# Optimization experiments

Hardware: AMD Instinct MI355X
Metric: run time of the kernel (lower is better)

Reference implementation:

```python
import jax, jax.numpy as jnp
import numpy as np

B, L, D = 1, 2048, 512
NL, N, K = 4, 16, 4
DI = 2 * D          # mamba expand=2
R = D // 16         # dt_rank = ceil(D/16)
H = 4 * D           # mlp hidden


def _ln(x, w, b, eps=1e-5):
    mu = x.mean(-1, keepdims=True)
    v = ((x - mu) ** 2).mean(-1, keepdims=True)
    return (x - mu) * jax.lax.rsqrt(v + eps) * w + b


def _rms(x, w, eps=1e-5):
    return x * jax.lax.rsqrt((x * x).mean(-1, keepdims=True) + eps) * w


def _ssm_scan(delta, Bm, Cm, u, A, Dp):
    # delta,u: (B,L,DI); Bm,Cm: (B,L,N); A: (DI,N); Dp: (DI,)
    def step(h, inp):
        d_t, b_t, c_t, u_t = inp                              # (B,DI),(B,N),(B,N),(B,DI)
        dA = jnp.exp(d_t[..., None] * A)                      # (B,DI,N)
        h = dA * h + (d_t * u_t)[..., None] * b_t[:, None, :]
        y = jnp.einsum('bdn,bn->bd', h, c_t)
        return h, y
    h0 = jnp.zeros((delta.shape[0], DI, N), delta.dtype)
    xs = (delta.swapaxes(0, 1), Bm.swapaxes(0, 1), Cm.swapaxes(0, 1), u.swapaxes(0, 1))
    _, ys = jax.lax.scan(step, h0, xs)
    return ys.swapaxes(0, 1) + u * Dp


def _mamba(h, in_w, cw, cb, xw, dtw, dtb, A_log, Dp, ow):
    xz = h @ in_w.T                                           # (B,L,2*DI)
    x, z = jnp.split(xz, 2, axis=-1)
    # causal depthwise conv1d, kernel K, left pad K-1
    xp = jnp.pad(x, ((0, 0), (K - 1, 0), (0, 0)))
    Ls = x.shape[1]
    x = sum(cw[:, k] * xp[:, k:k + Ls, :] for k in range(K)) + cb
    x = jax.nn.silu(x)
    dbc = x @ xw.T                                            # (B,L,R+2N)
    dt, Bm, Cm = dbc[..., :R], dbc[..., R:R + N], dbc[..., R + N:]
    delta = jax.nn.softplus(dt @ dtw.T + dtb)                 # (B,L,DI)
    A = -jnp.exp(A_log)                                       # (DI,N)
    y = _ssm_scan(delta, Bm, Cm, x, A, Dp)
    y = y * jax.nn.silu(z)
    return y @ ow.T


def _forward(hidden_states, ln1_w, ln1_b, in_proj_w, conv_w, conv_b, x_proj_w,
             dt_proj_w, dt_proj_b, A_log, D_param, out_proj_w, block_norm_w,
             norm_f_w, ln2_w, ln2_b, fc1_w, fc1_b, fc2_w, fc2_b):
    shortcut = hidden_states
    h = _ln(hidden_states, ln1_w, ln1_b)
    residual = None
    for i in range(in_proj_w.shape[0]):
        residual = h if residual is None else h + residual    # residual_in_fp32
        hn = _rms(residual, block_norm_w[i])                  # fused_add_norm prenorm
        h = _mamba(hn, in_proj_w[i], conv_w[i], conv_b[i], x_proj_w[i],
                   dt_proj_w[i], dt_proj_b[i], A_log[i], D_param[i], out_proj_w[i])
    h = _rms(h + residual, norm_f_w)                          # final rms_norm_fn
    h = shortcut + h
    x = _ln(h, ln2_w, ln2_b)
    x = jax.nn.gelu(x @ fc1_w.T + fc1_b)
    x = x @ fc2_w.T + fc2_b
    return h + x


def setup_inputs() -> dict:
    key = jax.random.key(0)
    ks = jax.random.split(key, 9)
    s = 0.02
    return {
        'hidden_states': jax.random.normal(ks[0], (B, L, D), jnp.float32),
        'ln1_w': jnp.ones((D,), jnp.float32),
        'ln1_b': jnp.zeros((D,), jnp.float32),
        'in_proj_w': jax.random.normal(ks[1], (NL, 2 * DI, D), jnp.float32) * s,
        'conv_w': jax.random.normal(ks[2], (NL, DI, K), jnp.float32) * 0.3,
        'conv_b': jnp.zeros((NL, DI), jnp.float32),
        'x_proj_w': jax.random.normal(ks[3], (NL, R + 2 * N, DI), jnp.float32) * s,
        'dt_proj_w': jax.random.normal(ks[4], (NL, DI, R), jnp.float32) * s,
        'dt_proj_b': jax.random.uniform(ks[5], (NL, DI), jnp.float32, -4.0, -2.0),
        'A_log': jnp.tile(jnp.log(jnp.arange(1, N + 1, dtype=jnp.float32)), (NL, DI, 1)),
        'D_param': jnp.ones((NL, DI), jnp.float32),
        'out_proj_w': jax.random.normal(ks[6], (NL, D, DI), jnp.float32) * s,
        'block_norm_w': jnp.ones((NL, D), jnp.float32),
        'norm_f_w': jnp.ones((D,), jnp.float32),
        'ln2_w': jnp.ones((D,), jnp.float32),
        'ln2_b': jnp.zeros((D,), jnp.float32),
        'fc1_w': jax.random.normal(ks[7], (H, D), jnp.float32) * s,
        'fc1_b': jnp.zeros((H,), jnp.float32),
        'fc2_w': jax.random.normal(ks[8], (D, H), jnp.float32) * s,
        'fc2_b': jnp.zeros((D,), jnp.float32),
    }


def reference(hidden_states, ln1_w, ln1_b, in_proj_w, conv_w, conv_b, x_proj_w,
              dt_proj_w, dt_proj_b, A_log, D_param, out_proj_w, block_norm_w,
              norm_f_w, ln2_w, ln2_b, fc1_w, fc1_b, fc2_w, fc2_b):
    return _forward(hidden_states, ln1_w, ln1_b, in_proj_w, conv_w, conv_b,
                    x_proj_w, dt_proj_w, dt_proj_b, A_log, D_param, out_proj_w,
                    block_norm_w, norm_f_w, ln2_w, ln2_b, fc1_w, fc1_b, fc2_w, fc2_b)
```

## Files before the change

kernel.cpp:

```cpp
#include <hip/hip_runtime.h>
#include <hip/hip_bf16.h>
#include <math.h>

#define L_SEQ 2048
#define Dm    512
#define DI    1024
#define Nst   16
#define Kc    4
#define Rr    32
#define NL    4
#define CH    128
#define LC    (L_SEQ / CH)

typedef __attribute__((ext_vector_type(8))) short bf16x8;
typedef __attribute__((ext_vector_type(4))) float f32x4;

__device__ __forceinline__ float act_softplus(float x) {
    return fmaxf(x, 0.f) + log1pf(__expf(-fabsf(x)));
}
__device__ __forceinline__ float act_gelu(float x) {
    float c = 0.7978845608028654f * (x + 0.044715f * x * x * x);
    float t = 1.f - 2.f / (__expf(2.f * c) + 1.f);
    return 0.5f * x * (1.f + t);
}
__device__ __forceinline__ float silu_(float x) {
    return x / (1.f + __expf(-x));
}
__device__ __forceinline__ ushort f2bf(float f) {
    union { float f; unsigned u; } c; c.f = f;
    unsigned r = c.u + 0x7fffu + ((c.u >> 16) & 1u);
    return (ushort)(r >> 16);
}
__device__ __forceinline__ float bf2f(ushort u) {
    union { unsigned u; float f; } c; c.u = ((unsigned)u) << 16;
    return c.f;
}
__device__ __forceinline__ float wave_sum(float v) {
    #pragma unroll
    for (int off = 32; off; off >>= 1) v += __shfl_xor(v, off);
    return v;
}

__global__ __launch_bounds__(256) void cast_all_kernel(
    const float* __restrict__ s0, ushort* __restrict__ d0, int n0,
    const float* __restrict__ s1, ushort* __restrict__ d1, int n1,
    const float* __restrict__ s2, ushort* __restrict__ d2, int n2,
    const float* __restrict__ s3, ushort* __restrict__ d3, int n3,
    const float* __restrict__ s4, ushort* __restrict__ d4, int n4_,
    const float* __restrict__ s5, ushort* __restrict__ d5, int n5)
{
    int i = blockIdx.x * 256 + threadIdx.x;
    const float* s; ushort* d;
    if (i < n0) { s = s0; d = d0; }
    else { i -= n0; if (i < n1) { s = s1; d = d1; }
    else { i -= n1; if (i < n2) { s = s2; d = d2; }
    else { i -= n2; if (i < n3) { s = s3; d = d3; }
    else { i -= n3; if (i < n4_) { s = s4; d = d4; }
    else { i -= n4_; if (i < n5) { s = s5; d = d5; } else return; } } } } }
    float4 v = ((const float4*)s)[i];
    ushort4 o;
    o.x = f2bf(v.x); o.y = f2bf(v.y); o.z = f2bf(v.z); o.w = f2bf(v.w);
    ((ushort4*)d)[i] = o;
}

__global__ __launch_bounds__(256) void ln_rms_kernel(const float* __restrict__ x,
    const float* __restrict__ w, const float* __restrict__ b,
    const float* __restrict__ rw, float* __restrict__ res,
    ushort* __restrict__ hn_bf)
{
    int lane = threadIdx.x & 63, wv = threadIdx.x >> 6;
    int row = blockIdx.x * 4 + wv;
    size_t base = (size_t)row * Dm + lane * 8;
    float v[8];
    *(float4*)(v)     = *(const float4*)(x + base);
    *(float4*)(v + 4) = *(const float4*)(x + base + 4);
    float s = 0.f, ss = 0.f;
    #pragma unroll
    for (int q = 0; q < 8; ++q) { s += v[q]; ss += v[q] * v[q]; }
    s = wave_sum(s); ss = wave_sum(ss);
    float mu = s * (1.f / Dm);
    float rs = rsqrtf(ss * (1.f / Dm) - mu * mu + 1e-5f);
    float wv8[8], bv8[8], rv8[8];
    *(float4*)(wv8)     = *(const float4*)(w + lane * 8);
    *(float4*)(wv8 + 4) = *(const float4*)(w + lane * 8 + 4);
    *(float4*)(bv8)     = *(const float4*)(b + lane * 8);
    *(float4*)(bv8 + 4) = *(const float4*)(b + lane * 8 + 4);
    *(float4*)(rv8)     = *(const float4*)(rw + lane * 8);
    *(float4*)(rv8 + 4) = *(const float4*)(rw + lane * 8 + 4);
    float o[8], ss2 = 0.f;
    #pragma unroll
    for (int q = 0; q < 8; ++q) {
        o[q] = (v[q] - mu) * rs * wv8[q] + bv8[q];
        ss2 += o[q] * o[q];
    }
    *(float4*)(res + base)     = *(float4*)(o);
    *(float4*)(res + base + 4) = *(float4*)(o + 4);
    ss2 = wave_sum(ss2);
    float rr = rsqrtf(ss2 * (1.f / Dm) + 1e-5f);
    bf16x8 hb;
    #pragma unroll
    for (int q = 0; q < 8; ++q) hb[q] = (short)f2bf(o[q] * rr * rv8[q]);
    *(bf16x8*)(hn_bf + base) = hb;
}

__global__ __launch_bounds__(256) void add_rms_kernel(const ushort* __restrict__ hb,
    float* __restrict__ res, const float* __restrict__ w, ushort* __restrict__ rms_out)
{
    int lane = threadIdx.x & 63, wv = threadIdx.x >> 6;
    int row = blockIdx.x * 4 + wv;
    size_t base = (size_t)row * Dm + lane * 8;
    bf16x8 hv = *(const bf16x8*)(hb + base);
    float v[8];
    *(float4*)(v)     = *(const float4*)(res + base);
    *(float4*)(v + 4) = *(const float4*)(res + base + 4);
    float ss = 0.f;
    #pragma unroll
    for (int q = 0; q < 8; ++q) {
        v[q] += bf2f((ushort)hv[q]);
        ss += v[q] * v[q];
    }
    *(float4*)(res + base)     = *(float4*)(v);
    *(float4*)(res + base + 4) = *(float4*)(v + 4);
    ss = wave_sum(ss);
    float rr = rsqrtf(ss * (1.f / Dm) + 1e-5f);
    float wv8[8];
    *(float4*)(wv8)     = *(const float4*)(w + lane * 8);
    *(float4*)(wv8 + 4) = *(const float4*)(w + lane * 8 + 4);
    bf16x8 ob;
    #pragma unroll
    for (int q = 0; q < 8; ++q) ob[q] = (short)f2bf(v[q] * rr * wv8[q]);
    *(bf16x8*)(rms_out + base) = ob;
}

__global__ __launch_bounds__(256) void final_ln2_kernel(const ushort* __restrict__ hb,
    const float* __restrict__ res, const float* __restrict__ shortcut,
    const float* __restrict__ wf, const float* __restrict__ w2,
    const float* __restrict__ b2, float* __restrict__ hout,
    ushort* __restrict__ yb16)
{
    int lane = threadIdx.x & 63, wv = threadIdx.x >> 6;
    int row = blockIdx.x * 4 + wv;
    size_t base = (size_t)row * Dm + lane * 8;
    bf16x8 hv = *(const bf16x8*)(hb + base);
    float v[8];
    *(float4*)(v)     = *(const float4*)(res + base);
    *(float4*)(v + 4) = *(const float4*)(res + base + 4);
    float ss = 0.f;
    #pragma unroll
    for (int q = 0; q < 8; ++q) {
        v[q] += bf2f((ushort)hv[q]);
        ss += v[q] * v[q];
    }
    ss = wave_sum(ss);
    float rs = rsqrtf(ss * (1.f / Dm) + 1e-5f);
    float sc[8], wf8[8];
    *(float4*)(sc)     = *(const float4*)(shortcut + base);
    *(float4*)(sc + 4) = *(const float4*)(shortcut + base + 4);
    *(float4*)(wf8)     = *(const float4*)(wf + lane * 8);
    *(float4*)(wf8 + 4) = *(const float4*)(wf + lane * 8 + 4);
    float t[8], s2 = 0.f, ss2 = 0.f;
    #pragma unroll
    for (int q = 0; q < 8; ++q) {
        t[q] = sc[q] + v[q] * rs * wf8[q];
        s2 += t[q]; ss2 += t[q] * t[q];
    }
    *(float4*)(hout + base)     = *(float4*)(t);
    *(float4*)(hout + base + 4) = *(float4*)(t + 4);
    s2 = wave_sum(s2); ss2 = wave_sum(ss2);
    float mu = s2 * (1.f / Dm);
    float rsig = rsqrtf(ss2 * (1.f / Dm) - mu * mu + 1e-5f);
    float w28[8], b28[8];
    *(float4*)(w28)     = *(const float4*)(w2 + lane * 8);
    *(float4*)(w28 + 4) = *(const float4*)(w2 + lane * 8 + 4);
    *(float4*)(b28)     = *(const float4*)(b2 + lane * 8);
    *(float4*)(b28 + 4) = *(const float4*)(b2 + lane * 8 + 4);
    bf16x8 ob;
    #pragma unroll
    for (int q = 0; q < 8; ++q) ob[q] = (short)f2bf((t[q] - mu) * rsig * w28[q] + b28[q]);
    *(bf16x8*)(yb16 + base) = ob;
}

template<int BM, int BN, int BK, int EPI>
__global__ __launch_bounds__(256) void gemm_mfma(
    const ushort* __restrict__ A, int lda,
    const ushort* __restrict__ W, int K,
    void* __restrict__ Cout, int ldc,
    const float* __restrict__ bias, const float* __restrict__ addsrc)
{
    constexpr int ROWB  = BK * 2;
    constexpr int SMASK = (ROWB / 16) - 1;
    constexpr int KK    = BK / 32;
    constexpr int WM = BM / 2, WN = BN / 2;
    constexpr int FM = WM / 16, FN = WN / 16;
    constexpr int ISS_A = (BM * ROWB) / 4096;
    constexpr int ISS_W = (BN * ROWB) / 4096;

    __shared__ __align__(16) ushort As[BM * BK];
    __shared__ __align__(16) ushort Ws[BN * BK];

    int tid = threadIdx.x;
    int wave = tid >> 6, lane = tid & 63;
    int wr = wave >> 1, wc = wave & 1;
    int l16 = lane & 15, lk = lane >> 4;
    int bm = blockIdx.y * BM, bn = blockIdx.x * BN;

    const ushort* srcA[ISS_A];
    const ushort* srcW[ISS_W];
    #pragma unroll
    for (int s = 0; s < ISS_A; ++s) {
        int off = s * 4096 + wave * 1024 + lane * 16;
        int row = off / ROWB;
        int slot = (off % ROWB) >> 4;
        int col = ((slot ^ (row & SMASK)) << 3);
        srcA[s] = A + (size_t)(bm + row) * lda + col;
    }
    #pragma unroll
    for (int s = 0; s < ISS_W; ++s) {
        int off = s * 4096 + wave * 1024 + lane * 16;
        int row = off / ROWB;
        int slot = (off % ROWB) >> 4;
        int col = ((slot ^ (row & SMASK)) << 3);
        srcW[s] = W + (size_t)(bn + row) * K + col;
    }
    int aoff[FM][KK], woff[FN][KK];
    #pragma unroll
    for (int i = 0; i < FM; ++i) {
        int row = wr * WM + i * 16 + l16;
        #pragma unroll
        for (int kk = 0; kk < KK; ++kk)
            aoff[i][kk] = row * BK + ((((kk << 2) | lk) ^ (row & SMASK)) << 3);
    }
    #pragma unroll
    for (int j = 0; j < FN; ++j) {
        int row = wc * WN + j * 16 + l16;
        #pragma unroll
        for (int kk = 0; kk < KK; ++kk)
            woff[j][kk] = row * BK + ((((kk << 2) | lk) ^ (row & SMASK)) << 3);
    }

    f32x4 acc[FM][FN] = {};

    for (int k0 = 0; k0 < K; k0 += BK) {
        #pragma unroll
        for (int s = 0; s < ISS_A; ++s)
            __builtin_amdgcn_global_load_lds(
                (const __attribute__((address_space(1))) void*)(srcA[s] + k0),
                (__attribute__((address_space(3))) void*)((char*)As + s * 4096 + wave * 1024),
                16, 0, 0);
        #pragma unroll
        for (int s = 0; s < ISS_W; ++s)
            __builtin_amdgcn_global_load_lds(
                (const __attribute__((address_space(1))) void*)(srcW[s] + k0),
                (__attribute__((address_space(3))) void*)((char*)Ws + s * 4096 + wave * 1024),
                16, 0, 0);
        __syncthreads();
        #pragma unroll
        for (int kk = 0; kk < KK; ++kk) {
            bf16x8 af[FM], wf[FN];
            #pragma unroll
            for (int i = 0; i < FM; ++i) af[i] = *(const bf16x8*)(As + aoff[i][kk]);
            #pragma unroll
            for (int j = 0; j < FN; ++j) wf[j] = *(const bf16x8*)(Ws + woff[j][kk]);
            #pragma unroll
            for (int i = 0; i < FM; ++i)
                #pragma unroll
                for (int j = 0; j < FN; ++j)
                    acc[i][j] = __builtin_amdgcn_mfma_f32_16x16x32_bf16(af[i], wf[j], acc[i][j], 0, 0, 0);
        }
        __syncthreads();
    }

    int orow0 = bm + wr * WM, ocol0 = bn + wc * WN;
    #pragma unroll
    for (int j = 0; j < FN; ++j) {
        int col = ocol0 + j * 16 + l16;
        float bj = 0.f;
        if constexpr (EPI == 2 || EPI == 4) bj = bias[col];
        #pragma unroll
        for (int i = 0; i < FM; ++i) {
            #pragma unroll
            for (int r = 0; r < 4; ++r) {
                int row = orow0 + i * 16 + lk * 4 + r;
                float v = acc[i][j][r];
                if constexpr (EPI == 1) {
                    ((ushort*)Cout)[(size_t)row * ldc + col] = f2bf(v);
                } else if constexpr (EPI == 2) {
                    ((ushort*)Cout)[(size_t)row * ldc + col] = f2bf(act_gelu(v + bj));
                } else if constexpr (EPI == 4) {
                    ((float*)Cout)[(size_t)row * ldc + col] = v + bj + addsrc[(size_t)row * ldc + col];
                }
            }
        }
    }
}

__global__ __launch_bounds__(256) void xproj_conv_kernel(
    const ushort* __restrict__ xz, const float* __restrict__ cw,
    const float* __restrict__ cb, const ushort* __restrict__ W,
    ushort* __restrict__ xc, float* __restrict__ part)
{
    constexpr int BM = 64, BN = 64, BK = 64;
    constexpr int ROWB  = BK * 2;
    constexpr int SMASK = (ROWB / 16) - 1;
    constexpr int KK    = BK / 32;
    constexpr int WM = 32, WN = 32, FM = 2, FN = 2;

    __shared__ __align__(16) ushort As[BM * BK];
    __shared__ __align__(16) ushort Ws[BN * BK];

    int tid = threadIdx.x;
    int wave = tid >> 6, lane = tid & 63;
    int wr = wave >> 1, wc = wave & 1;
    int l16 = lane & 15, lk = lane >> 4;
    int bm = blockIdx.y * BM;
    int z = blockIdx.z;
    int kbeg = z * (DI / 4);

    const ushort* srcW[2];
    #pragma unroll
    for (int s = 0; s < 2; ++s) {
        int off = s * 4096 + wave * 1024 + lane * 16;
        int row = off / ROWB;
        int slot = (off % ROWB) >> 4;
        int col = ((slot ^ (row & SMASK)) << 3);
        srcW[s] = W + (size_t)row * DI + kbeg + col;
    }
    int aoff[FM][KK], woff[FN][KK];
    #pragma unroll
    for (int i = 0; i < FM; ++i) {
        int row = wr * WM + i * 16 + l16;
        #pragma unroll
        for (int kk = 0; kk < KK; ++kk)
            aoff[i][kk] = row * BK + ((((kk << 2) | lk) ^ (row & SMASK)) << 3);
    }
    #pragma unroll
    for (int j = 0; j < FN; ++j) {
        int row = wc * WN + j * 16 + l16;
        #pragma unroll
        for (int kk = 0; kk < KK; ++kk)
            woff[j][kk] = row * BK + ((((kk << 2) | lk) ^ (row & SMASK)) << 3);
    }

    f32x4 acc[FM][FN] = {};

    for (int k0 = 0; k0 < DI / 4; k0 += BK) {
        #pragma unroll
        for (int s = 0; s < 2; ++s)
            __builtin_amdgcn_global_load_lds(
                (const __attribute__((address_space(1))) void*)(srcW[s] + k0),
                (__attribute__((address_space(3))) void*)((char*)Ws + s * 4096 + wave * 1024),
                16, 0, 0);
        #pragma unroll
        for (int s = 0; s < 2; ++s) {
            int off = s * 4096 + wave * 1024 + lane * 16;
            int row = off >> 7;
            int slot = (off >> 4) & 7;
            int t = bm + row;
            int dcol = kbeg + k0 + slot * 8;
            float a[8];
            float4 c4[8];
            #pragma unroll
            for (int q = 0; q < 8; ++q) {
                a[q] = cb[dcol + q];
                c4[q] = *(const float4*)(cw + (size_t)(dcol + q) * 4);
            }
            #pragma unroll
            for (int k = 0; k < 4; ++k) {
                int tt = t + k - 3;
                if (tt >= 0) {
                    bf16x8 xv = *(const bf16x8*)(xz + (size_t)tt * (2 * DI) + dcol);
                    #pragma unroll
                    for (int q = 0; q < 8; ++q) {
                        float wk = (k == 0) ? c4[q].x : (k == 1) ? c4[q].y
                                 : (k == 2) ? c4[q].z : c4[q].w;
                        a[q] = fmaf(wk, bf2f((ushort)xv[q]), a[q]);
                    }
                }
            }
            bf16x8 o;
            #pragma unroll
            for (int q = 0; q < 8; ++q) o[q] = (short)f2bf(silu_(a[q]));
            *(bf16x8*)(xc + (size_t)t * DI + dcol) = o;
            *(bf16x8*)(As + row * BK + ((slot ^ (row & SMASK)) << 3)) = o;
        }
        __syncthreads();
        #pragma unroll
        for (int kk = 0; kk < KK; ++kk) {
            bf16x8 af[FM], wf[FN];
            #pragma unroll
            for (int i = 0; i < FM; ++i) af[i] = *(const bf16x8*)(As + aoff[i][kk]);
            #pragma unroll
            for (int j = 0; j < FN; ++j) wf[j] = *(const bf16x8*)(Ws + woff[j][kk]);
            #pragma unroll
            for (int i = 0; i < FM; ++i)
                #pragma unroll
                for (int j = 0; j < FN; ++j)
                    acc[i][j] = __builtin_amdgcn_mfma_f32_16x16x32_bf16(af[i], wf[j], acc[i][j], 0, 0, 0);
        }
        __syncthreads();
    }

    float* coutf = part + (size_t)z * L_SEQ * 64;
    int orow0 = bm + wr * WM, ocol0 = wc * WN;
    #pragma unroll
    for (int j = 0; j < FN; ++j) {
        int col = ocol0 + j * 16 + l16;
        #pragma unroll
        for (int i = 0; i < FM; ++i)
            #pragma unroll
            for (int r = 0; r < 4; ++r) {
                int row = orow0 + i * 16 + lk * 4 + r;
                coutf[(size_t)row * 64 + col] = acc[i][j][r];
            }
    }
}

__global__ __launch_bounds__(256) void scan_chunk_kernel(
    const float* __restrict__ part, const ushort* __restrict__ u,
    const ushort* __restrict__ wdt, const float* __restrict__ dtb,
    const float* __restrict__ A_log,
    float* __restrict__ hend, float* __restrict__ aprod)
{
    __shared__ float sdt[LC][32];
    __shared__ float bsm[LC][16];
    int tid = threadIdx.x;
    int c = blockIdx.x;
    int d = blockIdx.y * 256 + tid;
    int t0 = c * LC;
    const int S = L_SEQ * 64;
    for (int i = tid; i < LC * 48; i += 256) {
        int tt = i / 48, cc = i % 48;
        int idx = (t0 + tt) * 64 + cc;
        float s = part[idx] + part[idx + S] + part[idx + 2 * S] + part[idx + 3 * S];
        if (cc < 32) sdt[tt][cc] = s; else bsm[tt][cc - 32] = s;
    }
    bf16x8 wd[4];
    #pragma unroll
    for (int p = 0; p < 4; ++p) wd[p] = *(const bf16x8*)(wdt + (size_t)d * 32 + p * 8);
    float bd = dtb[d];
    float A2[16];
    {
        float a[16];
        #pragma unroll
        for (int q = 0; q < 4; ++q)
            *(float4*)(a + q * 4) = ((const float4*)(A_log + (size_t)d * 16))[q];
        #pragma unroll
        for (int n = 0; n < 16; ++n)
            A2[n] = -__expf(a[n]) * 1.44269504f;
    }
    float h[16], ap[16];
    #pragma unroll
    for (int n = 0; n < 16; ++n) { h[n] = 0.f; ap[n] = 1.f; }
    __syncthreads();
    for (int tt = 0; tt < LC; ++tt) {
        int t = t0 + tt;
        float dtv = bd;
        #pragma unroll
        for (int p = 0; p < 4; ++p)
            #pragma unroll
            for (int e = 0; e < 8; ++e)
                dtv = fmaf(sdt[tt][p * 8 + e], bf2f((ushort)wd[p][e]), dtv);
        dtv = act_softplus(dtv);
        float du = dtv * bf2f(u[(size_t)t * DI + d]);
        #pragma unroll
        for (int n = 0; n < 16; ++n) {
            float dA = exp2f(dtv * A2[n]);
            h[n] = fmaf(dA, h[n], du * bsm[tt][n]);
            ap[n] *= dA;
        }
    }
    size_t base = ((size_t)c * DI + d) * 16;
    #pragma unroll
    for (int q = 0; q < 4; ++q) {
        ((float4*)(hend + base))[q]  = *(float4*)(h + q * 4);
        ((float4*)(aprod + base))[q] = *(float4*)(ap + q * 4);
    }
}

__global__ __launch_bounds__(64) void chunk_prefix_kernel(
    const float* __restrict__ hend, float* __restrict__ aprod_hin)
{
    int j = blockIdx.x * 64 + threadIdx.x;
    float h = 0.f;
    for (int cg = 0; cg < CH; cg += 8) {
        float ap[8], he[8];
        #pragma unroll
        for (int q = 0; q < 8; ++q) {
            size_t o = (size_t)(cg + q) * (DI * Nst) + j;
            ap[q] = aprod_hin[o]; he[q] = hend[o];
        }
        #pragma unroll
        for (int q = 0; q < 8; ++q) {
            size_t o = (size_t)(cg + q) * (DI * Nst) + j;
            aprod_hin[o] = h;
            h = fmaf(ap[q], h, he[q]);
        }
    }
}

__global__ __launch_bounds__(256) void scan_apply_kernel(
    const float* __restrict__ part, const ushort* __restrict__ u,
    const ushort* __restrict__ wdt, const float* __restrict__ dtb,
    const float* __restrict__ A_log, const float* __restrict__ Dp,
    const ushort* __restrict__ xz, const float* __restrict__ hin,
    ushort* __restrict__ y)
{
    __shared__ float sdt[LC][32];
    __shared__ float bsm[LC][16], csm[LC][16];
    int tid = threadIdx.x;
    int c = blockIdx.x;
    int d = blockIdx.y * 256 + tid;
    int t0 = c * LC;
    const int S = L_SEQ * 64;
    for (int i = tid; i < LC * 64; i += 256) {
        int tt = i >> 6, cc = i & 63;
        int idx = (t0 + tt) * 64 + cc;
        float s = part[idx] + part[idx + S] + part[idx + 2 * S] + part[idx + 3 * S];
        if (cc < 32) sdt[tt][cc] = s;
        else if (cc < 48) bsm[tt][cc - 32] = s;
        else csm[tt][cc - 48] = s;
    }
    bf16x8 wd[4];
    #pragma unroll
    for (int p = 0; p < 4; ++p) wd[p] = *(const bf16x8*)(wdt + (size_t)d * 32 + p * 8);
    float bd = dtb[d];
    float A2[16];
    {
        float a[16];
        #pragma unroll
        for (int q = 0; q < 4; ++q)
            *(float4*)(a + q * 4) = ((const float4*)(A_log + (size_t)d * 16))[q];
        #pragma unroll
        for (int n = 0; n < 16; ++n)
            A2[n] = -__expf(a[n]) * 1.44269504f;
    }
    float h[16];
    size_t base = ((size_t)c * DI + d) * 16;
    #pragma unroll
    for (int q = 0; q < 4; ++q)
        *(float4*)(h + q * 4) = ((const float4*)(hin + base))[q];
    float Dval = Dp[d];
    __syncthreads();
    for (int tt = 0; tt < LC; ++tt) {
        int t = t0 + tt;
        float dtv = bd;
        #pragma unroll
        for (int p = 0; p < 4; ++p)
            #pragma unroll
            for (int e = 0; e < 8; ++e)
                dtv = fmaf(sdt[tt][p * 8 + e], bf2f((ushort)wd[p][e]), dtv);
        dtv = act_softplus(dtv);
        float u_ = bf2f(u[(size_t)t * DI + d]);
        float du = dtv * u_;
        float acc = 0.f;
        #pragma unroll
        for (int n = 0; n < 16; ++n) {
            float dA = exp2f(dtv * A2[n]);
            h[n] = fmaf(dA, h[n], du * bsm[tt][n]);
            acc = fmaf(h[n], csm[tt][n], acc);
        }
        float zv = bf2f(xz[(size_t)t * (2 * DI) + DI + d]);
        y[(size_t)t * DI + d] = f2bf((acc + u_ * Dval) * silu_(zv));
    }
}

extern "C" void kernel_launch(void* const* d_in, const int* in_sizes, int n_in,
                              void* d_out, int out_size, void* d_ws, size_t ws_size,
                              hipStream_t stream)
{
    const float* hidden     = (const float*)d_in[0];
    const float* ln1_w      = (const float*)d_in[1];
    const float* ln1_b      = (const float*)d_in[2];
    const float* in_proj_w  = (const float*)d_in[3];
    const float* conv_w     = (const float*)d_in[4];
    const float* conv_b     = (const float*)d_in[5];
    const float* x_proj_w   = (const float*)d_in[6];
    const float* dt_proj_w  = (const float*)d_in[7];
    const float* dt_proj_b  = (const float*)d_in[8];
    const float* A_log      = (const float*)d_in[9];
    const float* D_param    = (const float*)d_in[10];
    const float* out_proj_w = (const float*)d_in[11];
    const float* block_norm_w = (const float*)d_in[12];
    const float* norm_f_w   = (const float*)d_in[13];
    const float* ln2_w      = (const float*)d_in[14];
    const float* ln2_b      = (const float*)d_in[15];
    const float* fc1_w      = (const float*)d_in[16];
    const float* fc1_b      = (const float*)d_in[17];
    const float* fc2_w      = (const float*)d_in[18];
    const float* fc2_b      = (const float*)d_in[19];

    char* P = (char*)d_ws;
    auto alloc = [&](size_t bytes) { char* r = P; P += (bytes + 255) & ~(size_t)255; return r; };
    float* hout   = (float*)alloc((size_t)L_SEQ * Dm * 4);
    float* res    = (float*)alloc((size_t)L_SEQ * Dm * 4);
    float* part   = (float*)alloc((size_t)4 * L_SEQ * 64 * 4);
    float* hend   = (float*)alloc((size_t)CH * DI * Nst * 4);
    float* aprod  = (float*)alloc((size_t)CH * DI * Nst * 4);
    ushort* h_bf  = (ushort*)alloc((size_t)L_SEQ * Dm * 2);
    ushort* hn_bf = (ushort*)alloc((size_t)L_SEQ * Dm * 2);
    ushort* xz_bf = (ushort*)alloc((size_t)L_SEQ * 2 * DI * 2);
    ushort* xc_bf = (ushort*)alloc((size_t)L_SEQ * DI * 2);
    ushort* yb_bf = (ushort*)alloc((size_t)L_SEQ * DI * 2);
    ushort* w_in  = (ushort*)alloc((size_t)NL * 2 * DI * Dm * 2);
    ushort* w_out = (ushort*)alloc((size_t)NL * Dm * DI * 2);
    ushort* w_x   = (ushort*)alloc((size_t)NL * 64 * DI * 2);
    ushort* w_dt  = (ushort*)alloc((size_t)NL * DI * Rr * 2);
    ushort* w_fc1 = (ushort*)alloc((size_t)(4 * Dm) * Dm * 2);
    ushort* w_fc2 = (ushort*)alloc((size_t)Dm * (4 * Dm) * 2);
    float* out  = (float*)d_out;

    {
        int n0 = NL * 2 * DI * Dm / 4, n1 = NL * Dm * DI / 4, n2 = NL * 64 * DI / 4;
        int n3 = NL * DI * Rr / 4, n4_ = 4 * Dm * Dm / 4, n5 = Dm * 4 * Dm / 4;
        int tot = n0 + n1 + n2 + n3 + n4_ + n5;
        cast_all_kernel<<<(tot + 255) / 256, 256, 0, stream>>>(
            in_proj_w, w_in, n0, out_proj_w, w_out, n1, x_proj_w, w_x, n2,
            dt_proj_w, w_dt, n3, fc1_w, w_fc1, n4_, fc2_w, w_fc2, n5);
    }

    ln_rms_kernel<<<L_SEQ / 4, 256, 0, stream>>>(hidden, ln1_w, ln1_b,
                                                 block_norm_w, res, hn_bf);

    dim3 gscan(CH, DI / 256);
    for (int i = 0; i < NL; ++i) {
        if (i) add_rms_kernel<<<L_SEQ / 4, 256, 0, stream>>>(h_bf, res,
                                                  block_norm_w + i * Dm, hn_bf);
        gemm_mfma<128, 128, 128, 1><<<dim3(2 * DI / 128, L_SEQ / 128), 256, 0, stream>>>(
            hn_bf, Dm, w_in + (size_t)i * 2 * DI * Dm, Dm, xz_bf, 2 * DI, nullptr, nullptr);
        xproj_conv_kernel<<<dim3(1, L_SEQ / 64, 4), 256, 0, stream>>>(
            xz_bf, conv_w + i * DI * Kc, conv_b + i * DI,
            w_x + (size_t)i * 64 * DI, xc_bf, part);
        scan_chunk_kernel<<<gscan, 256, 0, stream>>>(part, xc_bf,
                                        w_dt + (size_t)i * DI * Rr, dt_proj_b + i * DI,
                                        A_log + (size_t)i * DI * Nst, hend, aprod);
        chunk_prefix_kernel<<<(DI * Nst) / 64, 64, 0, stream>>>(hend, aprod);
        scan_apply_kernel<<<gscan, 256, 0, stream>>>(part, xc_bf,
                                        w_dt + (size_t)i * DI * Rr, dt_proj_b + i * DI,
                                        A_log + (size_t)i * DI * Nst,
                                        D_param + i * DI, xz_bf, aprod, yb_bf);
        gemm_mfma<64, 64, 128, 1><<<dim3(Dm / 64, L_SEQ / 64), 256, 0, stream>>>(
            yb_bf, DI, w_out + (size_t)i * Dm * DI, DI, h_bf, Dm, nullptr, nullptr);
    }

    final_ln2_kernel<<<L_SEQ / 4, 256, 0, stream>>>(h_bf, res, hidden, norm_f_w,
                                                ln2_w, ln2_b, hout, hn_bf);
    gemm_mfma<128, 128, 128, 2><<<dim3(2048 / 128, L_SEQ / 128), 256, 0, stream>>>(
        hn_bf, Dm, w_fc1, Dm, xz_bf, 2048, fc1_b, nullptr);
    gemm_mfma<64, 64, 128, 4><<<dim3(Dm / 64, L_SEQ / 64), 256, 0, stream>>>(
        xz_bf, 2048, w_fc2, 2048, out, Dm, fc2_b, hout);
}
```

Baseline: 476.7 us.

## Fuse LN into cast kernel, cache delta, raise x_proj split-K, shrink GEMM tiles

Merges the initial layernorm/RMS kernel into the weight-cast launch, which saves one kernel launch. The scan-chunk pass now writes softplus(delta) in bf16 so that scan_apply reads it instead of recomputing the dt projection. The x_proj split-K factor goes from 4 to 8 to spread the work over more blocks. GEMM tile N sizes are halved to raise block counts. The costs are extra partial-sum traffic, a delta buffer write and read, and bf16 rounding of delta in both scan passes.

New measurement: 390.5 us (median of 2 runs). -18.1%, faster.

```diff
diff --git a/kernel.cpp b/kernel.cpp
--- a/kernel.cpp
+++ b/kernel.cpp
@@ -11,6 +11,7 @@
 #define NL    4
 #define CH    128
 #define LC    (L_SEQ / CH)
+#define KSX   8
 
 typedef __attribute__((ext_vector_type(8))) short bf16x8;
 typedef __attribute__((ext_vector_type(4))) float f32x4;
@@ -41,15 +42,54 @@
     return v;
 }
 
-__global__ __launch_bounds__(256) void cast_all_kernel(
+__global__ __launch_bounds__(256) void setup_kernel(
     const float* __restrict__ s0, ushort* __restrict__ d0, int n0,
     const float* __restrict__ s1, ushort* __restrict__ d1, int n1,
     const float* __restrict__ s2, ushort* __restrict__ d2, int n2,
     const float* __restrict__ s3, ushort* __restrict__ d3, int n3,
     const float* __restrict__ s4, ushort* __restrict__ d4, int n4_,
-    const float* __restrict__ s5, ushort* __restrict__ d5, int n5)
-{
-    int i = blockIdx.x * 256 + threadIdx.x;
+    const float* __restrict__ s5, ushort* __restrict__ d5, int n5,
+    const float* __restrict__ x, const float* __restrict__ w,
+    const float* __restrict__ b, const float* __restrict__ rw,
+    float* __restrict__ res, ushort* __restrict__ hn_bf)
+{
+    if (blockIdx.x < 512) {
+        int lane = threadIdx.x & 63, wv = threadIdx.x >> 6;
+        int row = blockIdx.x * 4 + wv;
+        size_t base = (size_t)row * Dm + lane * 8;
+        float v[8];
+        *(float4*)(v)     = *(const float4*)(x + base);
+        *(float4*)(v + 4) = *(const float4*)(x + base + 4);
+        float s = 0.f, ss = 0.f;
+        #pragma unroll
+        for (int q = 0; q < 8; ++q) { s += v[q]; ss += v[q] * v[q]; }
+        s = wave_sum(s); ss = wave_sum(ss);
+        float mu = s * (1.f / Dm);
+        float rs = rsqrtf(ss * (1.f / Dm) - mu * mu + 1e-5f);
+        float wv8[8], bv8[8], rv8[8];
+        *(float4*)(wv8)     = *(const float4*)(w + lane * 8);
+        *(float4*)(wv8 + 4) = *(const float4*)(w + lane * 8 + 4);
+        *(float4*)(bv8)     = *(const float4*)(b + lane * 8);
+        *(float4*)(bv8 + 4) = *(const float4*)(b + lane * 8 + 4);
+        *(float4*)(rv8)     = *(const float4*)(rw + lane * 8);
+        *(float4*)(rv8 + 4) = *(const float4*)(rw + lane * 8 + 4);
+        float o[8], ss2 = 0.f;
+        #pragma unroll
+        for (int q = 0; q < 8; ++q) {
+            o[q] = (v[q] - mu) * rs * wv8[q] + bv8[q];
+            ss2 += o[q] * o[q];
+        }
+        *(float4*)(res + base)     = *(float4*)(o);
+        *(float4*)(res + base + 4) = *(float4*)(o + 4);
+        ss2 = wave_sum(ss2);
+        float rr = rsqrtf(ss2 * (1.f / Dm) + 1e-5f);
+        bf16x8 hb;
+        #pragma unroll
+        for (int q = 0; q < 8; ++q) hb[q] = (short)f2bf(o[q] * rr * rv8[q]);
+        *(bf16x8*)(hn_bf + base) = hb;
+        return;
+    }
+    int i = (blockIdx.x - 512) * 256 + threadIdx.x;
     const float* s; ushort* d;
     if (i < n0) { s = s0; d = d0; }
     else { i -= n0; if (i < n1) { s = s1; d = d1; }
@@ -63,46 +103,6 @@
     ((ushort4*)d)[i] = o;
 }
 
-__global__ __launch_bounds__(256) void ln_rms_kernel(const float* __restrict__ x,
-    const float* __restrict__ w, const float* __restrict__ b,
-    const float* __restrict__ rw, float* __restrict__ res,
-    ushort* __restrict__ hn_bf)
-{
-    int lane = threadIdx.x & 63, wv = threadIdx.x >> 6;
-    int row = blockIdx.x * 4 + wv;
-    size_t base = (size_t)row * Dm + lane * 8;
-    float v[8];
-    *(float4*)(v)     = *(const float4*)(x + base);
-    *(float4*)(v + 4) = *(const float4*)(x + base + 4);
-    float s = 0.f, ss = 0.f;
-    #pragma unroll
-    for (int q = 0; q < 8; ++q) { s += v[q]; ss += v[q] * v[q]; }
-    s = wave_sum(s); ss = wave_sum(ss);
-    float mu = s * (1.f / Dm);
-    float rs = rsqrtf(ss * (1.f / Dm) - mu * mu + 1e-5f);
-    float wv8[8], bv8[8], rv8[8];
-    *(float4*)(wv8)     = *(const float4*)(w + lane * 8);
-    *(float4*)(wv8 + 4) = *(const float4*)(w + lane * 8 + 4);
-    *(float4*)(bv8)     = *(const float4*)(b + lane * 8);
-    *(float4*)(bv8 + 4) = *(const float4*)(b + lane * 8 + 4);
-    *(float4*)(rv8)     = *(const float4*)(rw + lane * 8);
-    *(float4*)(rv8 + 4) = *(const float4*)(rw + lane * 8 + 4);
-    float o[8], ss2 = 0.f;
-    #pragma unroll
-    for (int q = 0; q < 8; ++q) {
-        o[q] = (v[q] - mu) * rs * wv8[q] + bv8[q];
-        ss2 += o[q] * o[q];
-    }
-    *(float4*)(res + base)     = *(float4*)(o);
-    *(float4*)(res + base + 4) = *(float4*)(o + 4);
-    ss2 = wave_sum(ss2);
-    float rr = rsqrtf(ss2 * (1.f / Dm) + 1e-5f);
-    bf16x8 hb;
-    #pragma unroll
-    for (int q = 0; q < 8; ++q) hb[q] = (short)f2bf(o[q] * rr * rv8[q]);
-    *(bf16x8*)(hn_bf + base) = hb;
-}
-
 __global__ __launch_bounds__(256) void add_rms_kernel(const ushort* __restrict__ hb,
     float* __restrict__ res, const float* __restrict__ w, ushort* __restrict__ rms_out)
 {
@@ -314,7 +314,7 @@
     int l16 = lane & 15, lk = lane >> 4;
     int bm = blockIdx.y * BM;
     int z = blockIdx.z;
-    int kbeg = z * (DI / 4);
+    int kbeg = z * (DI / KSX);
 
     const ushort* srcW[2];
     #pragma unroll
@@ -343,7 +343,7 @@
 
     f32x4 acc[FM][FN] = {};
 
-    for (int k0 = 0; k0 < DI / 4; k0 += BK) {
+    for (int k0 = 0; k0 < DI / KSX; k0 += BK) {
         #pragma unroll
         for (int s = 0; s < 2; ++s)
             __builtin_amdgcn_global_load_lds(
@@ -419,7 +419,8 @@
     const float* __restrict__ part, const ushort* __restrict__ u,
     const ushort* __restrict__ wdt, const float* __restrict__ dtb,
     const float* __restrict__ A_log,
-    float* __restrict__ hend, float* __restrict__ aprod)
+    float* __restrict__ hend, float* __restrict__ aprod,
+    ushort* __restrict__ delta_bf)
 {
     __shared__ float sdt[LC][32];
     __shared__ float bsm[LC][16];
@@ -431,7 +432,9 @@
     for (int i = tid; i < LC * 48; i += 256) {
         int tt = i / 48, cc = i % 48;
         int idx = (t0 + tt) * 64 + cc;
-        float s = part[idx] + part[idx + S] + part[idx + 2 * S] + part[idx + 3 * S];
+        float s = 0.f;
+        #pragma unroll
+        for (int p = 0; p < KSX; ++p) s += part[idx + p * S];
         if (cc < 32) sdt[tt][cc] = s; else bsm[tt][cc - 32] = s;
     }
     bf16x8 wd[4];
@@ -460,11 +463,13 @@
             #pragma unroll
             for (int e = 0; e < 8; ++e)
                 dtv = fmaf(sdt[tt][p * 8 + e], bf2f((ushort)wd[p][e]), dtv);
-        dtv = act_softplus(dtv);
-        float du = dtv * bf2f(u[(size_t)t * DI + d]);
+        ushort dbf = f2bf(act_softplus(dtv));
+        delta_bf[(size_t)t * DI + d] = dbf;
+        float dt_ = bf2f(dbf);
+        float du = dt_ * bf2f(u[(size_t)t * DI + d]);
         #pragma unroll
         for (int n = 0; n < 16; ++n) {
-            float dA = exp2f(dtv * A2[n]);
+            float dA = exp2f(dt_ * A2[n]);
             h[n] = fmaf(dA, h[n], du * bsm[tt][n]);
             ap[n] *= dA;
         }
@@ -499,31 +504,25 @@
 }
 
 __global__ __launch_bounds__(256) void scan_apply_kernel(
-    const float* __restrict__ part, const ushort* __restrict__ u,
-    const ushort* __restrict__ wdt, const float* __restrict__ dtb,
-    const float* __restrict__ A_log, const float* __restrict__ Dp,
-    const ushort* __restrict__ xz, const float* __restrict__ hin,
-    ushort* __restrict__ y)
-{
-    __shared__ float sdt[LC][32];
+    const float* __restrict__ part, const ushort* __restrict__ delta,
+    const ushort* __restrict__ u, const float* __restrict__ A_log,
+    const float* __restrict__ Dp, const ushort* __restrict__ xz,
+    const float* __restrict__ hin, ushort* __restrict__ y)
+{
     __shared__ float bsm[LC][16], csm[LC][16];
     int tid = threadIdx.x;
     int c = blockIdx.x;
     int d = blockIdx.y * 256 + tid;
     int t0 = c * LC;
     const int S = L_SEQ * 64;
-    for (int i = tid; i < LC * 64; i += 256) {
-        int tt = i >> 6, cc = i & 63;
-        int idx = (t0 + tt) * 64 + cc;
-        float s = part[idx] + part[idx + S] + part[idx + 2 * S] + part[idx + 3 * S];
-        if (cc < 32) sdt[tt][cc] = s;
-        else if (cc < 48) bsm[tt][cc - 32] = s;
-        else csm[tt][cc - 48] = s;
-    }
-    bf16x8 wd[4];
-    #pragma unroll
-    for (int p = 0; p < 4; ++p) wd[p] = *(const bf16x8*)(wdt + (size_t)d * 32 + p * 8);
-    float bd = dtb[d];
+    for (int i = tid; i < LC * 32; i += 256) {
+        int tt = i >> 5, k = i & 31;
+        int idx = (t0 + tt) * 64 + 32 + k;
+        float s = 0.f;
+        #pragma unroll
+        for (int p = 0; p < KSX; ++p) s += part[idx + p * S];
+        if (k < 16) bsm[tt][k] = s; else csm[tt][k - 16] = s;
+    }
     float A2[16];
     {
         float a[16];
@@ -543,19 +542,13 @@
     __syncthreads();
     for (int tt = 0; tt < LC; ++tt) {
         int t = t0 + tt;
-        float dtv = bd;
-        #pragma unroll
-        for (int p = 0; p < 4; ++p)
-            #pragma unroll
-            for (int e = 0; e < 8; ++e)
-                dtv = fmaf(sdt[tt][p * 8 + e], bf2f((ushort)wd[p][e]), dtv);
-        dtv = act_softplus(dtv);
-        float u_ = bf2f(u[(size_t)t * DI + d]);
-        float du = dtv * u_;
+        float dt_ = bf2f(delta[(size_t)t * DI + d]);
+        float u_  = bf2f(u[(size_t)t * DI + d]);
+        float du  = dt_ * u_;
         float acc = 0.f;
         #pragma unroll
         for (int n = 0; n < 16; ++n) {
-            float dA = exp2f(dtv * A2[n]);
+            float dA = exp2f(dt_ * A2[n]);
             h[n] = fmaf(dA, h[n], du * bsm[tt][n]);
             acc = fmaf(h[n], csm[tt][n], acc);
         }
@@ -593,10 +586,11 @@
     auto alloc = [&](size_t bytes) { char* r = P; P += (bytes + 255) & ~(size_t)255; return r; };
     float* hout   = (float*)alloc((size_t)L_SEQ * Dm * 4);
     float* res    = (float*)alloc((size_t)L_SEQ * Dm * 4);
-    float* part   = (float*)alloc((size_t)4 * L_SEQ * 64 * 4);
+    float* part   = (float*)alloc((size_t)KSX * L_SEQ * 64 * 4);
     float* hend   = (float*)alloc((size_t)CH * DI * Nst * 4);
     float* aprod  = (float*)alloc((size_t)CH * DI * Nst * 4);
     ushort* h_bf  = (ushort*)alloc((size_t)L_SEQ * Dm * 2);
+    ushort* delta_bf = (ushort*)alloc((size_t)L_SEQ * DI * 2);
     ushort* hn_bf = (ushort*)alloc((size_t)L_SEQ * Dm * 2);
     ushort* xz_bf = (ushort*)alloc((size_t)L_SEQ * 2 * DI * 2);
     ushort* xc_bf = (ushort*)alloc((size_t)L_SEQ * DI * 2);
@@ -613,39 +607,37 @@
         int n0 = NL * 2 * DI * Dm / 4, n1 = NL * Dm * DI / 4, n2 = NL * 64 * DI / 4;
         int n3 = NL * DI * Rr / 4, n4_ = 4 * Dm * Dm / 4, n5 = Dm * 4 * Dm / 4;
         int tot = n0 + n1 + n2 + n3 + n4_ + n5;
-        cast_all_kernel<<<(tot + 255) / 256, 256, 0, stream>>>(
+        int grid = 512 + (tot + 255) / 256;
+        setup_kernel<<<grid, 256, 0, stream>>>(
             in_proj_w, w_in, n0, out_proj_w, w_out, n1, x_proj_w, w_x, n2,
-            dt_proj_w, w_dt, n3, fc1_w, w_fc1, n4_, fc2_w, w_fc2, n5);
-    }
-
-    ln_rms_kernel<<<L_SEQ / 4, 256, 0, stream>>>(hidden, ln1_w, ln1_b,
-                                                 block_norm_w, res, hn_bf);
+            dt_proj_w, w_dt, n3, fc1_w, w_fc1, n4_, fc2_w, w_fc2, n5,
+            hidden, ln1_w, ln1_b, block_norm_w, res, hn_bf);
+    }
 
     dim3 gscan(CH, DI / 256);
     for (int i = 0; i < NL; ++i) {
         if (i) add_rms_kernel<<<L_SEQ / 4, 256, 0, stream>>>(h_bf, res,
                                                   block_norm_w + i * Dm, hn_bf);
-        gemm_mfma<128, 128, 128, 1><<<dim3(2 * DI / 128, L_SEQ / 128), 256, 0, stream>>>(
+        gemm_mfma<128, 64, 128, 1><<<dim3(2 * DI / 64, L_SEQ / 128), 256, 0, stream>>>(
             hn_bf, Dm, w_in + (size_t)i * 2 * DI * Dm, Dm, xz_bf, 2 * DI, nullptr, nullptr);
-        xproj_conv_kernel<<<dim3(1, L_SEQ / 64, 4), 256, 0, stream>>>(
+        xproj_conv_kernel<<<dim3(1, L_SEQ / 64, KSX), 256, 0, stream>>>(
             xz_bf, conv_w + i * DI * Kc, conv_b + i * DI,
             w_x + (size_t)i * 64 * DI, xc_bf, part);
         scan_chunk_kernel<<<gscan, 256, 0, stream>>>(part, xc_bf,
                                         w_dt + (size_t)i * DI * Rr, dt_proj_b + i * DI,
-                                        A_log + (size_t)i * DI * Nst, hend, aprod);
+                                        A_log + (size_t)i * DI * Nst, hend, aprod, delta_bf);
         chunk_prefix_kernel<<<(DI * Nst) / 64, 64, 0, stream>>>(hend, aprod);
-        scan_apply_kernel<<<gscan, 256, 0, stream>>>(part, xc_bf,
-                                        w_dt + (size_t)i * DI * Rr, dt_proj_b + i * DI,
+        scan_apply_kernel<<<gscan, 256, 0, stream>>>(part, delta_bf, xc_bf,
                                         A_log + (size_t)i * DI * Nst,
                                         D_param + i * DI, xz_bf, aprod, yb_bf);
-        gemm_mfma<64, 64, 128, 1><<<dim3(Dm / 64, L_SEQ / 64), 256, 0, stream>>>(
+        gemm_mfma<64, 32, 128, 1><<<dim3(Dm / 32, L_SEQ / 64), 256, 0, stream>>>(
             yb_bf, DI, w_out + (size_t)i * Dm * DI, DI, h_bf, Dm, nullptr, nullptr);
     }
 
     final_ln2_kernel<<<L_SEQ / 4, 256, 0, stream>>>(h_bf, res, hidden, norm_f_w,
                                                 ln2_w, ln2_b, hout, hn_bf);
-    gemm_mfma<128, 128, 128, 2><<<dim3(2048 / 128, L_SEQ / 128), 256, 0, stream>>>(
+    gemm_mfma<128, 64, 128, 2><<<dim3(2048 / 64, L_SEQ / 128), 256, 0, stream>>>(
         hn_bf, Dm, w_fc1, Dm, xz_bf, 2048, fc1_b, nullptr);
-    gemm_mfma<64, 64, 128, 4><<<dim3(Dm / 64, L_SEQ / 64), 256, 0, stream>>>(
+    gemm_mfma<64, 32, 128, 4><<<dim3(Dm / 32, L_SEQ / 64), 256, 0, stream>>>(
         xz_bf, 2048, w_fc2, 2048, out, Dm, fc2_b, hout);
 }
```
